# Kernel tuning notes

Measured on AMD Instinct MI355X. Metric: run time of the kernel, lower is better.

## Reference

```python
import jax, jax.numpy as jnp
import numpy as np

CHANNELS_CHOICE = np.array([8, 16, 24, 32, 40, 48, 56, 64])
MAX_C = 64
B, H, W_SP = 128, 32, 32
N_EDGES = 6
# edge list per intermediate node: (edge_weight_index, source_node_index)
EDGES = [[(0, 0)], [(1, 0), (2, 1)], [(3, 0), (4, 1), (5, 2)]]


def setup_inputs() -> dict:
    key = jax.random.key(0)
    k1, k2, k3, k4 = jax.random.split(key, 4)
    inputs = jax.random.normal(k1, (B, MAX_C, H, W_SP), dtype=jnp.float32)
    alphas1 = jax.random.uniform(k2, (8,), dtype=jnp.float32)  # input-width arch weights
    alphas2 = jax.random.uniform(k3, (8,), dtype=jnp.float32)  # output-width arch weights
    # shared master 3x3 conv weight per edge (OIHW)
    W = jax.random.normal(k4, (N_EDGES, MAX_C, MAX_C, 3, 3), dtype=jnp.float32) * 0.05
    return {"inputs": inputs, "alphas1": alphas1, "alphas2": alphas2, "W": W}


def _channel_scale(alphas1, alphas2, dtype):
    # mask[c, i] = 1 if channel c is inside width choice CHANNELS_CHOICE[i]
    mask = (jnp.arange(MAX_C)[:, None] < jnp.asarray(CHANNELS_CHOICE)[None, :]).astype(dtype)  # [64, 8]
    a_in = mask @ alphas1   # [64] cumulative input-channel weight
    a_out = mask @ alphas2  # [64] cumulative output-channel weight
    return a_out[:, None] * a_in[None, :]  # [64, 64]


def _edge(x, w, scale):
    # weighted-combi of all (c1, c2) channel-sliced sub-convs == one conv with scaled weight
    w_eff = w * scale[:, :, None, None]
    return jax.lax.conv_general_dilated(
        jax.nn.relu(x), w_eff, window_strides=(1, 1), padding="SAME",
        dimension_numbers=("NCHW", "OIHW", "NCHW"))


def reference(inputs, alphas1, alphas2, W):
    scale = _channel_scale(alphas1, alphas2, inputs.dtype)
    nodes = [inputs]
    for node_edges in EDGES:
        feat = 0.0
        for l, src in node_edges:
            feat = feat + _edge(nodes[src], W[l], scale)
        nodes.append(feat)
    return nodes[-1]
```

## Files before the change

kernel.cpp:

```cpp
#include <hip/hip_runtime.h>
#include <hip/hip_bf16.h>


typedef __bf16 bf16x8 __attribute__((ext_vector_type(8)));
typedef float floatx4 __attribute__((ext_vector_type(4)));
typedef unsigned int uint32;
typedef uint32 u32x4 __attribute__((ext_vector_type(4)));

#define PADW 34
#define PIMG (PADW * PADW)
#define ROWB (PADW * 64 * 2)
#define A_LDS (10 * ROWB)
#define A_CHUNKS (A_LDS / 16)
#define A_TAIL (A_CHUNKS - 10 * 256)
#define TAPB (64 * 64 * 2)
#define B_LDS (9 * TAPB)
#define SMEM_BYTES (A_LDS + B_LDS)

__device__ __forceinline__ void gld16(const char* g, char* l) {
    __builtin_amdgcn_global_load_lds(
        (const __attribute__((address_space(1))) uint32*)g,
        (__attribute__((address_space(3))) uint32*)l, 16, 0, 0);
}

__global__ __launch_bounds__(256) void pre_kernel(
    const float* __restrict__ in, const float* __restrict__ a1,
    const float* __restrict__ a2, const float* __restrict__ W,
    __hip_bfloat16* __restrict__ wt, __hip_bfloat16* __restrict__ wtR,
    __hip_bfloat16* __restrict__ r0, __hip_bfloat16* __restrict__ r1,
    __hip_bfloat16* __restrict__ r2) {
    __shared__ float tile[32][65];
    int blk = blockIdx.x;
    int tid = threadIdx.x;

    if (blk < 864) {
        int idx = blk * 256 + tid;
        int i = idx & 63;
        int o = (idx >> 6) & 63;
        int rest = idx >> 12;
        int t = rest % 9;
        int l = rest / 9;
        int ji = i >> 3, jo = o >> 3;
        float ain = 0.f, aout = 0.f;
#pragma unroll
        for (int j = 0; j < 8; ++j) {
            ain  += (j >= ji) ? a1[j] : 0.f;
            aout += (j >= jo) ? a2[j] : 0.f;
        }
        float v = W[(size_t)((l * 64 + o) * 64 + i) * 9 + t] * ain * aout;
        int os = ((o & 3) << 4) + (o >> 2);
        size_t e = (size_t)(l * 9 + t) * 4096 + os * 64 +
                   ((((i >> 3) ^ (os & 7)) << 3) + (i & 7));
        __hip_bfloat16 bv = __float2bfloat16(v);
        wt[e] = bv;
        int n  = os >> 4, c15 = os & 15;
        int q  = i >> 5, quad = (i >> 3) & 3, ee = i & 7;
        int ln = (quad << 4) + c15;
        size_t e2 = (size_t)(l * 9 + t) * 4096 + (((q << 2) + n) << 9) +
                    (ln << 3) + ee;
        wtR[e2] = bv;
    } else if (blk < 992) {
        int b = blk - 864;
        __hip_bfloat16* bufs[3] = {r0, r1, r2};
#pragma unroll
        for (int f = 0; f < 3; ++f) {
            uint32* buf = (uint32*)(bufs[f] + (size_t)b * PIMG * 64);
            for (int idx = tid; idx < 132 * 32; idx += 256) {
                int slot = idx >> 5, u = idx & 31;
                int yy, xx;
                if (slot < 34)      { yy = 0;  xx = slot; }
                else if (slot < 68) { yy = 33; xx = slot - 34; }
                else { int s2 = slot - 68; yy = 1 + (s2 >> 1); xx = (s2 & 1) * 33; }
                buf[(size_t)(yy * PADW + xx) * 32 + u] = 0u;
            }
        }
    } else {
        int rb = blk - 992;
        int b = rb >> 5, y = rb & 31;
        int x = tid & 31, c0 = tid >> 5;
        const float* ip = in + ((size_t)b * 64 * 32 + y) * 32 + x;
#pragma unroll
        for (int cc = 0; cc < 8; ++cc) {
            int c = cc * 8 + c0;
            tile[x][c] = fmaxf(ip[(size_t)c * 1024], 0.f);
        }
        __syncthreads();
        int j = tid & 7, xq = tid >> 3;
        int p = (b * PADW + y + 1) * PADW + 1 + xq;
        alignas(16) __hip_bfloat16 hv[8];
#pragma unroll
        for (int k = 0; k < 8; ++k)
            hv[k] = __float2bfloat16(tile[xq][j * 8 + k]);
        *(uint4*)((char*)r0 + (size_t)p * 128 + ((j ^ (p & 7)) << 4)) =
            *(const uint4*)hv;
    }
}

#define ZERO4(A_)                                                        \
    _Pragma("unroll") for (int m_ = 0; m_ < 4; ++m_)                     \
    _Pragma("unroll") for (int n_ = 0; n_ < 4; ++n_)                     \
        A_[m_][n_] = (floatx4){0.f, 0.f, 0.f, 0.f};

template <int MODE>
__global__ __launch_bounds__(256, 1) void conv_k(
    const __hip_bfloat16* __restrict__ Asrc,
    const __hip_bfloat16* __restrict__ wt,
    const __hip_bfloat16* __restrict__ wtR,
    __hip_bfloat16* __restrict__ nodeOut, float* __restrict__ finalOut,
    __hip_bfloat16* __restrict__ p2, __hip_bfloat16* __restrict__ p3) {
    extern __shared__ char smem[];
    char* smemB = smem + A_LDS;
    int tid = threadIdx.x;
    int wv = tid >> 6, lane = tid & 63;
    int quad = lane >> 4, l15 = lane & 15;
    int blk = blockIdx.x;
    int b = blk >> 2, y0 = (blk & 3) << 3;
    const int Rb = b * PADW + y0;
    const size_t aOff = (size_t)Rb * PADW * 128;
    const size_t pbase = ((size_t)blk * 256 + tid) << 7;

    auto stage_A = [&]() {
        const char* gA = (const char*)Asrc + aOff;
#pragma unroll
        for (int it = 0; it < 11; ++it) {
            int c = it * 256 + tid;
            if (it < 10 || tid < A_TAIL)
                gld16(gA + (size_t)c * 16, smem + (it * 256 + wv * 64) * 16);
        }
    };
    auto stage_B = [&](int l) {
        const char* gB = (const char*)wt + (size_t)l * 9 * TAPB;
#pragma unroll
        for (int it = 0; it < 18; ++it) {
            int c = it * 256 + tid;
            gld16(gB + (size_t)c * 16, smemB + (it * 256 + wv * 64) * 16);
        }
    };
    auto ldA = [&](int tl, int q, bf16x8 (&dst)[4]) {
        const int ky = tl / 3, kx = tl % 3;
#pragma unroll
        for (int m = 0; m < 4; ++m) {
            int arow = 2 * wv + (m >> 1) + ky;
            int apx  = ((m & 1) << 4) + l15 + kx;
            int R = Rb + arow;
            int slot = ((q << 2) + quad) ^ ((2 * R + apx) & 7);
            dst[m] = *(const bf16x8*)(smem + arow * ROWB + apx * 128 +
                                      slot * 16);
        }
    };
    auto ldB = [&](int tl, int q, bf16x8 (&dst)[4]) {
#pragma unroll
        for (int n = 0; n < 4; ++n) {
            int o = (n << 4) + l15;
            int slot = ((q << 2) + quad) ^ (l15 & 7);
            dst[n] = *(const bf16x8*)(smemB + tl * TAPB + o * 128 +
                                      slot * 16);
        }
    };
    auto init_p = [&](floatx4 (&acc)[4][4], const __hip_bfloat16* p) {
#pragma unroll
        for (int c = 0; c < 8; ++c) {
            alignas(16) __hip_bfloat16 hv[8];
            *(uint4*)hv = *(const uint4*)((const char*)p + pbase + c * 16);
#pragma unroll
            for (int k = 0; k < 8; ++k) {
                int j = c * 8 + k;
                acc[j >> 4][(j >> 2) & 3][j & 3] = __bfloat162float(hv[k]);
            }
        }
    };
    auto epi_p = [&](floatx4 (&acc)[4][4], __hip_bfloat16* p) {
#pragma unroll
        for (int c = 0; c < 8; ++c) {
            alignas(16) __hip_bfloat16 hv[8];
#pragma unroll
            for (int k = 0; k < 8; ++k) {
                int j = c * 8 + k;
                hv[k] = __float2bfloat16(acc[j >> 4][(j >> 2) & 3][j & 3]);
            }
            *(uint4*)((char*)p + pbase + c * 16) = *(const uint4*)hv;
        }
    };
    auto epi_node = [&](floatx4 (&acc)[4][4], __hip_bfloat16* dst) {
#pragma unroll
        for (int m = 0; m < 4; ++m) {
            int row = y0 + 2 * wv + (m >> 1);
#pragma unroll
            for (int r = 0; r < 4; ++r) {
                int x = ((m & 1) << 4) + (quad << 2) + r;
                int p = (b * PADW + row + 1) * PADW + x + 1;
                alignas(8) __hip_bfloat16 hv[4];
#pragma unroll
                for (int n = 0; n < 4; ++n)
                    hv[n] = __float2bfloat16(fmaxf(acc[m][n][r], 0.f));
                char* d8 = (char*)dst + (size_t)p * 128 +
                           ((((l15 >> 1) ^ (p & 7)) << 4) + ((l15 & 1) << 3));
                *(uint2*)d8 = *(const uint2*)hv;
            }
        }
    };
    auto paired_pass = [&](int lR, floatx4 (&accL)[4][4],
                           floatx4 (&accR)[4][4]) {
        const char* gR = (const char*)wtR + (size_t)lR * 9 * TAPB;
        auto ldBg = [&](int t, u32x4 (&dst)[8]) {
#pragma unroll
            for (int f = 0; f < 8; ++f)
                dst[f] = *(const __attribute__((address_space(1))) u32x4*)
                    (gR + (size_t)t * TAPB + (f << 10) + (lane << 4));
        };
        bf16x8 Af[2][4], Bf[2][4];
        u32x4 Bb[2][8];
        ldBg(0, Bb[0]);
        ldA(0, 0, Af[0]);
        ldB(0, 0, Bf[0]);
#pragma unroll
        for (int st = 0; st < 18; ++st) {
            const int pb = st & 1, t = st >> 1;
            if (st < 17) {
                const int nt = (st + 1) >> 1, nq = (st + 1) & 1;
                ldA(nt, nq, Af[pb ^ 1]);
                ldB(nt, nq, Bf[pb ^ 1]);
            }
            if (pb == 0 && t < 8) ldBg(t + 1, Bb[(t + 1) & 1]);
            __builtin_amdgcn_s_setprio(1);
#pragma unroll
            for (int m = 0; m < 4; ++m)
#pragma unroll
                for (int n = 0; n < 4; ++n)
                    accL[m][n] = __builtin_amdgcn_mfma_f32_16x16x32_bf16(
                        Af[pb][m], Bf[pb][n], accL[m][n], 0, 0, 0);
#pragma unroll
            for (int n = 0; n < 4; ++n) {
                bf16x8 Br = __builtin_bit_cast(bf16x8,
                                               Bb[t & 1][(pb << 2) + n]);
#pragma unroll
                for (int m = 0; m < 4; ++m)
                    accR[m][n] = __builtin_amdgcn_mfma_f32_16x16x32_bf16(
                        Af[pb][m], Br, accR[m][n], 0, 0, 0);
            }
            __builtin_amdgcn_s_setprio(0);
        }
    };
    auto single_pass = [&](floatx4 (&acc)[4][4]) {
        bf16x8 fA[2][4], fB[2][4];
        ldA(0, 0, fA[0]);
        ldB(0, 0, fB[0]);
#pragma unroll
        for (int st = 0; st < 18; ++st) {
            const int pb = st & 1;
            if (st < 17) {
                const int nt = (st + 1) >> 1, nq = (st + 1) & 1;
                ldA(nt, nq, fA[pb ^ 1]);
                ldB(nt, nq, fB[pb ^ 1]);
            }
            __builtin_amdgcn_s_setprio(1);
#pragma unroll
            for (int m = 0; m < 4; ++m)
#pragma unroll
                for (int n = 0; n < 4; ++n)
                    acc[m][n] = __builtin_amdgcn_mfma_f32_16x16x32_bf16(
                        fA[pb][m], fB[pb][n], acc[pb ? m : m][n], 0, 0, 0);
            __builtin_amdgcn_s_setprio(0);
        }
    };

    if constexpr (MODE == 1) {
        stage_A();
        stage_B(0);
        __syncthreads();
        floatx4 aT[4][4], aX[4][4];
        ZERO4(aT); ZERO4(aX);
        paired_pass(1, aT, aX);
        epi_node(aT, nodeOut);
        epi_p(aX, p2);
        __syncthreads();
        stage_B(3);
        __syncthreads();
        floatx4 aY[4][4];
        ZERO4(aY);
        single_pass(aY);
        epi_p(aY, p3);
    } else if constexpr (MODE == 2) {
        stage_A();
        stage_B(2);
        __syncthreads();
        floatx4 aX[4][4], aY[4][4];
        init_p(aX, p2);
        init_p(aY, p3);
        paired_pass(4, aX, aY);
        epi_node(aX, nodeOut);
        epi_p(aY, p3);
    } else {
        stage_A();
        stage_B(5);
        __syncthreads();
        floatx4 aY[4][4];
        init_p(aY, p3);
        single_pass(aY);
#pragma unroll
        for (int m = 0; m < 4; ++m) {
            int row = y0 + 2 * wv + (m >> 1);
#pragma unroll
            for (int n = 0; n < 4; ++n) {
                int o = (l15 << 2) + n;
                *(floatx4*)(finalOut +
                            (((size_t)b * 64 + o) * 32 + row) * 32 +
                            ((m & 1) << 4) + (quad << 2)) = aY[m][n];
            }
        }
    }
}

extern "C" void kernel_launch(void* const* d_in, const int* in_sizes, int n_in,
                              void* d_out, int out_size, void* d_ws,
                              size_t ws_size, hipStream_t stream) {
    const float* inputs  = (const float*)d_in[0];
    const float* alphas1 = (const float*)d_in[1];
    const float* alphas2 = (const float*)d_in[2];
    const float* W       = (const float*)d_in[3];
    char* ws = (char*)d_ws;

    __hip_bfloat16* wt  = (__hip_bfloat16*)(ws);
    __hip_bfloat16* wtR = (__hip_bfloat16*)(ws + ((size_t)1 << 19));
    __hip_bfloat16* r0 = (__hip_bfloat16*)(ws + ((size_t)1 << 20));
    __hip_bfloat16* r1 = (__hip_bfloat16*)(ws + ((size_t)20 << 20));
    __hip_bfloat16* r2 = (__hip_bfloat16*)(ws + ((size_t)40 << 20));
    __hip_bfloat16* p2 = (__hip_bfloat16*)(ws + ((size_t)60 << 20));
    __hip_bfloat16* p3 = (__hip_bfloat16*)(ws + ((size_t)80 << 20));
    float* out = (float*)d_out;

    (void)hipFuncSetAttribute((const void*)conv_k<1>,
                              hipFuncAttributeMaxDynamicSharedMemorySize,
                              SMEM_BYTES);
    (void)hipFuncSetAttribute((const void*)conv_k<2>,
                              hipFuncAttributeMaxDynamicSharedMemorySize,
                              SMEM_BYTES);
    (void)hipFuncSetAttribute((const void*)conv_k<3>,
                              hipFuncAttributeMaxDynamicSharedMemorySize,
                              SMEM_BYTES);

    pre_kernel<<<864 + 128 + 4096, 256, 0, stream>>>(
        inputs, alphas1, alphas2, W, wt, wtR, r0, r1, r2);
    conv_k<1><<<512, 256, SMEM_BYTES, stream>>>(r0, wt, wtR, r1, nullptr,
                                                p2, p3);
    conv_k<2><<<512, 256, SMEM_BYTES, stream>>>(r1, wt, wtR, r2, nullptr,
                                                p2, p3);
    conv_k<3><<<512, 256, SMEM_BYTES, stream>>>(r2, wt, wtR, nullptr, out,
                                                p2, p3);
}
```

Measured before the change: 180.0 us.

## Stream conv weights through double-buffered LDS tap groups to fit two blocks per CU

Instead of staging all nine 3x3 weight taps into LDS up front, the kernel now loads weights in groups of two taps into a double buffer and prefetches the next group while MFMAs run on the current one. This shrinks the LDS footprint from about 10 rows plus 9 taps to 10 rows plus 4 taps, and the launch bounds are raised to allow two blocks per CU. The goal is higher occupancy and overlap of weight loads with compute, which also removes the exposed stage_B stall between passes. The cost is extra __syncthreads per group and tighter register limits, which could cause spills given the large accumulator arrays.

```diff
diff --git a/kernel.cpp b/kernel.cpp
--- a/kernel.cpp
+++ b/kernel.cpp
@@ -6,6 +6,7 @@
 typedef float floatx4 __attribute__((ext_vector_type(4)));
 typedef unsigned int uint32;
 typedef uint32 u32x4 __attribute__((ext_vector_type(4)));
+#define AS1 __attribute__((address_space(1)))
 
 #define PADW 34
 #define PIMG (PADW * PADW)
@@ -14,13 +15,13 @@
 #define A_CHUNKS (A_LDS / 16)
 #define A_TAIL (A_CHUNKS - 10 * 256)
 #define TAPB (64 * 64 * 2)
-#define B_LDS (9 * TAPB)
-#define SMEM_BYTES (A_LDS + B_LDS)
+#define GRPB (2 * TAPB)
+#define SMEM_BYTES (A_LDS + 2 * GRPB)
 
 __device__ __forceinline__ void gld16(const char* g, char* l) {
     __builtin_amdgcn_global_load_lds(
-        (const __attribute__((address_space(1))) uint32*)g,
-        (__attribute__((address_space(3))) uint32*)l, 16, 0, 0);
+        (const AS1 uint32*)g, (__attribute__((address_space(3))) uint32*)l,
+        16, 0, 0);
 }
 
 __global__ __launch_bounds__(256) void pre_kernel(
@@ -102,7 +103,7 @@
         A_[m_][n_] = (floatx4){0.f, 0.f, 0.f, 0.f};
 
 template <int MODE>
-__global__ __launch_bounds__(256, 1) void conv_k(
+__global__ __launch_bounds__(256, 2) void conv_k(
     const __hip_bfloat16* __restrict__ Asrc,
     const __hip_bfloat16* __restrict__ wt,
     const __hip_bfloat16* __restrict__ wtR,
@@ -128,12 +129,12 @@
                 gld16(gA + (size_t)c * 16, smem + (it * 256 + wv * 64) * 16);
         }
     };
-    auto stage_B = [&](int l) {
-        const char* gB = (const char*)wt + (size_t)l * 9 * TAPB;
-#pragma unroll
-        for (int it = 0; it < 18; ++it) {
+    auto stage_Bgrp = [&](int l, int tap0, int nt, char* dst) {
+        const char* gB = (const char*)wt + ((size_t)l * 9 + tap0) * TAPB;
+#pragma unroll
+        for (int it = 0; it < 2 * nt; ++it) {
             int c = it * 256 + tid;
-            gld16(gB + (size_t)c * 16, smemB + (it * 256 + wv * 64) * 16);
+            gld16(gB + (size_t)c * 16, dst + (it * 256 + wv * 64) * 16);
         }
     };
     auto ldA = [&](int tl, int q, bf16x8 (&dst)[4]) {
@@ -148,12 +149,12 @@
                                       slot * 16);
         }
     };
-    auto ldB = [&](int tl, int q, bf16x8 (&dst)[4]) {
+    auto ldBb = [&](const char* bufB, int lt, int q, bf16x8 (&dst)[4]) {
 #pragma unroll
         for (int n = 0; n < 4; ++n) {
             int o = (n << 4) + l15;
             int slot = ((q << 2) + quad) ^ (l15 & 7);
-            dst[n] = *(const bf16x8*)(smemB + tl * TAPB + o * 128 +
+            dst[n] = *(const bf16x8*)(bufB + lt * TAPB + o * 128 +
                                       slot * 16);
         }
     };
@@ -199,29 +200,31 @@
             }
         }
     };
-    auto paired_pass = [&](int lR, floatx4 (&accL)[4][4],
-                           floatx4 (&accR)[4][4]) {
+    auto paired_group = [&](const char* bufB, int lR, int t0, int nt,
+                            floatx4 (&accL)[4][4], floatx4 (&accR)[4][4]) {
         const char* gR = (const char*)wtR + (size_t)lR * 9 * TAPB;
-        auto ldBg = [&](int t, u32x4 (&dst)[8]) {
-#pragma unroll
-            for (int f = 0; f < 8; ++f)
-                dst[f] = *(const __attribute__((address_space(1))) u32x4*)
-                    (gR + (size_t)t * TAPB + (f << 10) + (lane << 4));
-        };
+        u32x4 Bb[2][8];
+#pragma unroll
+        for (int f = 0; f < 8; ++f)
+            Bb[0][f] = *(const AS1 u32x4*)(gR + (size_t)t0 * TAPB +
+                                           (f << 10) + (lane << 4));
         bf16x8 Af[2][4], Bf[2][4];
-        u32x4 Bb[2][8];
-        ldBg(0, Bb[0]);
-        ldA(0, 0, Af[0]);
-        ldB(0, 0, Bf[0]);
-#pragma unroll
-        for (int st = 0; st < 18; ++st) {
-            const int pb = st & 1, t = st >> 1;
-            if (st < 17) {
-                const int nt = (st + 1) >> 1, nq = (st + 1) & 1;
-                ldA(nt, nq, Af[pb ^ 1]);
-                ldB(nt, nq, Bf[pb ^ 1]);
-            }
-            if (pb == 0 && t < 8) ldBg(t + 1, Bb[(t + 1) & 1]);
+        ldA(t0, 0, Af[0]);
+        ldBb(bufB, 0, 0, Bf[0]);
+#pragma unroll
+        for (int st = 0; st < 2 * nt; ++st) {
+            const int pb = st & 1, lt = st >> 1;
+            if (st + 1 < 2 * nt) {
+                ldA(t0 + ((st + 1) >> 1), (st + 1) & 1, Af[pb ^ 1]);
+                ldBb(bufB, (st + 1) >> 1, (st + 1) & 1, Bf[pb ^ 1]);
+            }
+            if (pb == 0 && lt + 1 < nt) {
+#pragma unroll
+                for (int f = 0; f < 8; ++f)
+                    Bb[(lt + 1) & 1][f] = *(const AS1 u32x4*)
+                        (gR + (size_t)(t0 + lt + 1) * TAPB + (f << 10) +
+                         (lane << 4));
+            }
             __builtin_amdgcn_s_setprio(1);
 #pragma unroll
             for (int m = 0; m < 4; ++m)
@@ -232,7 +235,7 @@
 #pragma unroll
             for (int n = 0; n < 4; ++n) {
                 bf16x8 Br = __builtin_bit_cast(bf16x8,
-                                               Bb[t & 1][(pb << 2) + n]);
+                                               Bb[lt & 1][(pb << 2) + n]);
 #pragma unroll
                 for (int m = 0; m < 4; ++m)
                     accR[m][n] = __builtin_amdgcn_mfma_f32_16x16x32_bf16(
@@ -241,17 +244,17 @@
             __builtin_amdgcn_s_setprio(0);
         }
     };
-    auto single_pass = [&](floatx4 (&acc)[4][4]) {
-        bf16x8 fA[2][4], fB[2][4];
-        ldA(0, 0, fA[0]);
-        ldB(0, 0, fB[0]);
-#pragma unroll
-        for (int st = 0; st < 18; ++st) {
+    auto single_group = [&](const char* bufB, int t0, int nt,
+                            floatx4 (&acc)[4][4]) {
+        bf16x8 Af[2][4], Bf[2][4];
+        ldA(t0, 0, Af[0]);
+        ldBb(bufB, 0, 0, Bf[0]);
+#pragma unroll
+        for (int st = 0; st < 2 * nt; ++st) {
             const int pb = st & 1;
-            if (st < 17) {
-                const int nt = (st + 1) >> 1, nq = (st + 1) & 1;
-                ldA(nt, nq, fA[pb ^ 1]);
-                ldB(nt, nq, fB[pb ^ 1]);
+            if (st + 1 < 2 * nt) {
+                ldA(t0 + ((st + 1) >> 1), (st + 1) & 1, Af[pb ^ 1]);
+                ldBb(bufB, (st + 1) >> 1, (st + 1) & 1, Bf[pb ^ 1]);
             }
             __builtin_amdgcn_s_setprio(1);
 #pragma unroll
@@ -259,44 +262,74 @@
 #pragma unroll
                 for (int n = 0; n < 4; ++n)
                     acc[m][n] = __builtin_amdgcn_mfma_f32_16x16x32_bf16(
-                        fA[pb][m], fB[pb][n], acc[pb ? m : m][n], 0, 0, 0);
+                        Af[pb][m], Bf[pb][n], acc[m][n], 0, 0, 0);
             __builtin_amdgcn_s_setprio(0);
         }
     };
 
     if constexpr (MODE == 1) {
         stage_A();
-        stage_B(0);
+        stage_Bgrp(0, 0, 2, smemB);
         __syncthreads();
         floatx4 aT[4][4], aX[4][4];
         ZERO4(aT); ZERO4(aX);
-        paired_pass(1, aT, aX);
+#pragma unroll
+        for (int g = 0; g < 5; ++g) {
+            char* cur = smemB + (g & 1) * GRPB;
+            char* nxt = smemB + ((g + 1) & 1) * GRPB;
+            if (g < 4) stage_Bgrp(0, 2 * (g + 1), (g + 1 == 4) ? 1 : 2, nxt);
+            else       stage_Bgrp(3, 0, 2, nxt);
+            __builtin_amdgcn_sched_barrier(0);
+            paired_group(cur, 1, 2 * g, (g == 4) ? 1 : 2, aT, aX);
+            __syncthreads();
+        }
         epi_node(aT, nodeOut);
         epi_p(aX, p2);
-        __syncthreads();
-        stage_B(3);
-        __syncthreads();
         floatx4 aY[4][4];
         ZERO4(aY);
-        single_pass(aY);
+#pragma unroll
+        for (int g = 0; g < 5; ++g) {
+            char* cur = smemB + ((5 + g) & 1) * GRPB;
+            char* nxt = smemB + ((6 + g) & 1) * GRPB;
+            if (g < 4) stage_Bgrp(3, 2 * (g + 1), (g + 1 == 4) ? 1 : 2, nxt);
+            __builtin_amdgcn_sched_barrier(0);
+            single_group(cur, 2 * g, (g == 4) ? 1 : 2, aY);
+            if (g < 4) __syncthreads();
+        }
         epi_p(aY, p3);
     } else if constexpr (MODE == 2) {
         stage_A();
-        stage_B(2);
+        stage_Bgrp(2, 0, 2, smemB);
         __syncthreads();
         floatx4 aX[4][4], aY[4][4];
         init_p(aX, p2);
         init_p(aY, p3);
-        paired_pass(4, aX, aY);
+#pragma unroll
+        for (int g = 0; g < 5; ++g) {
+            char* cur = smemB + (g & 1) * GRPB;
+            char* nxt = smemB + ((g + 1) & 1) * GRPB;
+            if (g < 4) stage_Bgrp(2, 2 * (g + 1), (g + 1 == 4) ? 1 : 2, nxt);
+            __builtin_amdgcn_sched_barrier(0);
+            paired_group(cur, 4, 2 * g, (g == 4) ? 1 : 2, aX, aY);
+            if (g < 4) __syncthreads();
+        }
         epi_node(aX, nodeOut);
         epi_p(aY, p3);
     } else {
         stage_A();
-        stage_B(5);
+        stage_Bgrp(5, 0, 2, smemB);
         __syncthreads();
         floatx4 aY[4][4];
         init_p(aY, p3);
-        single_pass(aY);
+#pragma unroll
+        for (int g = 0; g < 5; ++g) {
+            char* cur = smemB + (g & 1) * GRPB;
+            char* nxt = smemB + ((g + 1) & 1) * GRPB;
+            if (g < 4) stage_Bgrp(5, 2 * (g + 1), (g + 1 == 4) ? 1 : 2, nxt);
+            __builtin_amdgcn_sched_barrier(0);
+            single_group(cur, 2 * g, (g == 4) ? 1 : 2, aY);
+            if (g < 4) __syncthreads();
+        }
 #pragma unroll
         for (int m = 0; m < 4; ++m) {
             int row = y0 + 2 * wv + (m >> 1);
```

New measurement: 232.5 us. 29.1% more time.
